# Optimization experiments

Measured on AMD Instinct MI355X. Metric: run time of the kernel, lower is better.

The kernel has to match this reference:

```python
import jax, jax.numpy as jnp
import numpy as np

B, T, D, H = 32, 1024, 1024, 1024


def gru_cell(x, h, W_ih, W_hh, b_ih, b_hh):
    # torch.nn.GRUCell math; gate order (r, z, n)
    gi = x @ W_ih.T + b_ih          # [B, 3H]
    gh = h @ W_hh.T + b_hh          # [B, 3H]
    i_r, i_z, i_n = jnp.split(gi, 3, axis=-1)
    h_r, h_z, h_n = jnp.split(gh, 3, axis=-1)
    r = jax.nn.sigmoid(i_r + h_r)
    z = jax.nn.sigmoid(i_z + h_z)
    n = jnp.tanh(i_n + r * h_n)
    return (1.0 - z) * n + z * h


def setup_inputs() -> dict:
    key = jax.random.key(0)
    k = jax.random.split(key, 6)
    scale = np.float32(1.0 / np.sqrt(H))  # torch GRUCell init range
    x = jax.random.normal(k[0], (B, T, D), jnp.float32)
    seg = jax.random.randint(k[1], (B, T), 0, 2).astype(jnp.int32)
    W_ih = jax.random.normal(k[2], (3 * H, D), jnp.float32) * scale
    W_hh = jax.random.normal(k[3], (3 * H, H), jnp.float32) * scale
    b_ih = jax.random.normal(k[4], (3 * H,), jnp.float32) * scale
    b_hh = jax.random.normal(k[5], (3 * H,), jnp.float32) * scale
    return {"x": x, "W_ih": W_ih, "W_hh": W_hh, "b_ih": b_ih, "b_hh": b_hh, "seg": seg}


def reference(x, W_ih, W_hh, b_ih, b_hh, seg):
    # apply_rnn_pack: GRUCell scan with segment-masked reset + ragged pack.
    segf = seg.astype(x.dtype)

    def step(h, inp):
        xt, st = inp                      # xt [B,D], st [B]
        h_new = gru_cell(xt, h, W_ih, W_hh, b_ih, b_hh)
        h_next = st[:, None] * h_new      # reset hidden where seg==0
        return h_next, h_new              # emit pre-reset hidden

    h0 = jnp.zeros((B, H), x.dtype)
    xs = (jnp.swapaxes(x, 0, 1), jnp.swapaxes(segf, 0, 1))
    _, hs = jax.lax.scan(step, h0, xs)    # hs [T,B,H]
    hs = jnp.swapaxes(hs, 0, 1)           # [B,T,H]

    # Pack: write h at step t into slot (#emits before t) iff seg[b,t]==0.
    emit = seg == 0                       # [B,T]
    pos = jnp.cumsum(emit, axis=1) - 1    # destination slot for emitted steps
    pos = jnp.where(emit, pos, T)         # route non-emitted steps to pad slot
    out = jnp.zeros((B, T + 1, H), x.dtype)
    b_idx = jnp.arange(B)[:, None]
    out = out.at[b_idx, pos].set(hs)
    out = out[:, :T]                      # [B,T,H], ragged-padded with zeros
    counts = emit.sum(axis=1)             # per-sample packed lengths (idx)
    return out, counts
```

## Files before the change

### kernel.cpp

```cpp
#include <hip/hip_runtime.h>

#define NB 32
#define NT 1024
#define ND 1024
#define NH 1024
#define G3 3072
#define MROWS 32768
#define HROWS 16512
#define GSROWS 32896
#define TAILG 256

typedef __bf16 bf16x8 __attribute__((ext_vector_type(8)));
typedef float f32x4 __attribute__((ext_vector_type(4)));
typedef unsigned short u16x8 __attribute__((ext_vector_type(8)));
typedef unsigned short u16x4 __attribute__((ext_vector_type(4)));

__device__ __forceinline__ float b2f(unsigned short u){
  union { unsigned int i; float f; } v; v.i = ((unsigned int)u) << 16; return v.f;
}
__device__ __forceinline__ unsigned short f2b(float f){
  union { float f; unsigned int i; } v; v.f = f;
  unsigned int r = (v.i + 0x7FFFu + ((v.i >> 16) & 1u)) >> 16;
  return (unsigned short)r;
}
__device__ __forceinline__ float sigm(float x){ return 1.0f / (1.0f + __expf(-x)); }
__device__ __forceinline__ float tanh_(float x){ return 2.0f / (1.0f + __expf(-2.0f * x)) - 1.0f; }

__device__ __forceinline__ void g2l16(const void* g, void* l){
  __builtin_amdgcn_global_load_lds((__attribute__((address_space(1))) void*)g,
                                   (__attribute__((address_space(3))) void*)l, 16, 0, 0);
}

__global__ __launch_bounds__(256) void k_setup(const float* __restrict__ wih,
    const float* __restrict__ whh, const float* __restrict__ x,
    unsigned short* __restrict__ wih_b, unsigned short* __restrict__ whh_b,
    unsigned short* __restrict__ x_b, int has_xb, f32x4* __restrict__ outv, int out_n4){
  int i0 = blockIdx.x * 256 + threadIdx.x;
  int stride = gridDim.x * 256;
  f32x4 z = {0.f, 0.f, 0.f, 0.f};
  for (int j = i0; j < out_n4; j += stride) __builtin_nontemporal_store(z, &outv[j]);
  int nw4 = (G3 * ND) / 4;
  for (int j = i0; j < nw4; j += stride){
    f32x4 a = ((const f32x4*)wih)[j];
    f32x4 b = ((const f32x4*)whh)[j];
    u16x4 ua = {f2b(a[0]), f2b(a[1]), f2b(a[2]), f2b(a[3])};
    u16x4 ub = {f2b(b[0]), f2b(b[1]), f2b(b[2]), f2b(b[3])};
    ((u16x4*)wih_b)[j] = ua;
    ((u16x4*)whh_b)[j] = ub;
  }
  if (has_xb){
    int nx4 = (MROWS * ND) / 4;
    for (int j = i0; j < nx4; j += stride){
      f32x4 a = ((const f32x4*)x)[j];
      u16x4 u = {f2b(a[0]), f2b(a[1]), f2b(a[2]), f2b(a[3])};
      ((u16x4*)x_b)[j] = u;
    }
  }
}

__global__ __launch_bounds__(1024) void k_segbuild(const int* __restrict__ seg,
    int* __restrict__ ugi, int* __restrict__ uout, int* __restrict__ ulen,
    int* __restrict__ nseg_b,
    int* __restrict__ sgi, int* __restrict__ sout, int* __restrict__ slen,
    int* __restrict__ cnt_ge, int* __restrict__ base_g,
    unsigned int* __restrict__ perm, unsigned int* __restrict__ bar,
    float* __restrict__ counts_out){
  __shared__ int hist[1025];
  __shared__ int sufx[1024];
  __shared__ int pref[1024];
  __shared__ int offs[1025];
  int tid = threadIdx.x;
  int wave = tid >> 6, lane = tid & 63;
  if (tid == 0) *bar = 0u;

  for (int b = wave; b < NB; b += 16){
    int prev = -1;
    int zc = 0;
    for (int c = 0; c < 16; ++c){
      int t = c * 64 + lane;
      int v = seg[b * NT + t];
      unsigned long long mask = __ballot(v == 0);
      unsigned long long below = mask & ((1ULL << lane) - 1ULL);
      if (v == 0){
        int pz = below ? (c * 64 + (63 - __clzll((long long)below))) : prev;
        int eidx = zc + __popcll(below);
        int slot = b * NT + eidx;
        ugi[slot]  = b * NT + (pz + 1);
        uout[slot] = b * NT + eidx;
        ulen[slot] = t - pz;
      }
      if (mask) prev = c * 64 + (63 - __clzll((long long)mask));
      zc += __popcll(mask);
    }
    if (lane == 0){ nseg_b[b] = zc; counts_out[b] = (float)zc; }
  }
  __syncthreads();
  for (int i = tid; i <= 1024; i += 1024) hist[i] = 0;
  __syncthreads();
  for (int s = tid; s < NB * NT; s += 1024){
    int b = s >> 10, j = s & 1023;
    if (j < nseg_b[b]) atomicAdd(&hist[ulen[s]], 1);
  }
  __syncthreads();
  if (tid < 1024) sufx[tid] = hist[tid + 1];
  __syncthreads();
  for (int off = 1; off < 1024; off <<= 1){
    int v = (tid + off < 1024) ? sufx[tid + off] : 0;
    __syncthreads();
    sufx[tid] += v;
    __syncthreads();
  }
  cnt_ge[tid + 1] = sufx[tid];
  if (tid == 0){ cnt_ge[0] = sufx[0]; cnt_ge[1025] = 0; }
  offs[tid] = sufx[tid];
  if (tid == 0) offs[1024] = 0;
  pref[tid] = sufx[tid];
  __syncthreads();
  for (int off = 1; off < 1024; off <<= 1){
    int v = (tid >= off) ? pref[tid - off] : 0;
    __syncthreads();
    pref[tid] += v;
    __syncthreads();
  }
  base_g[tid + 1] = pref[tid];
  if (tid == 0){ base_g[0] = 0; base_g[1025] = pref[1023]; }
  __syncthreads();
  for (int s = tid; s < NB * NT; s += 1024){
    int b = s >> 10, j = s & 1023;
    if (j < nseg_b[b]){
      int len = ulen[s];
      int p = atomicAdd(&offs[len], 1);
      sgi[p] = ugi[s]; sout[p] = uout[s]; slen[p] = len;
    }
  }
  for (int m = tid; m < MROWS; m += 1024) perm[m] = 0xFFFFFFFFu;
  __syncthreads();
  int nseg = cnt_ge[1];
  for (int p = tid; p < nseg; p += 1024){
    int src = sgi[p];
    int len = slen[p];
    perm[src] = (unsigned int)p;
    for (int kk = 1; kk < len; ++kk)
      perm[src + kk] = (unsigned int)(pref[kk - 1] + p);
  }
}

__global__ __launch_bounds__(256, 2) void k_gi_gemm(const float* __restrict__ x,
    const unsigned short* __restrict__ x_b, const unsigned short* __restrict__ wih_b,
    const float* __restrict__ b_ih, const unsigned int* __restrict__ perm,
    unsigned short* __restrict__ gs, int use_xb){
  __shared__ unsigned short Alds[128 * 64];
  __shared__ unsigned short Blds[128 * 64];
  int tid = threadIdx.x;
  int w = tid >> 6, lane = tid & 63;
  int mtile = blockIdx.x / 24, ntile = blockIdx.x % 24;
  int m0 = mtile * 128, n0 = ntile * 128;
  int mh = (w >> 1) * 64, nh = (w & 1) * 64;
  int lrow = lane >> 3;
  int lcol = 8 * ((lane & 7) ^ lrow);
  f32x4 acc[4][4];
#pragma unroll
  for (int i = 0; i < 4; ++i)
#pragma unroll
    for (int j = 0; j < 4; ++j) acc[i][j] = (f32x4){0.f, 0.f, 0.f, 0.f};

  for (int kc = 0; kc < 16; ++kc){
    __syncthreads();
    if (use_xb){
#pragma unroll
      for (int p = 0; p < 4; ++p){
        int s = w * 4 + p;
        g2l16(x_b + (size_t)(m0 + s * 8 + lrow) * ND + kc * 64 + lcol, &Alds[s * 512]);
      }
    } else {
#pragma unroll
      for (int p = 0; p < 4; ++p){
        int e = (p * 256 + tid) * 8;
        int r = e >> 6, c = e & 63;
        const float* src = x + (size_t)(m0 + r) * ND + kc * 64 + c;
        f32x4 f0 = *(const f32x4*)src;
        f32x4 f1 = *(const f32x4*)(src + 4);
        u16x8 u;
        u[0]=f2b(f0[0]); u[1]=f2b(f0[1]); u[2]=f2b(f0[2]); u[3]=f2b(f0[3]);
        u[4]=f2b(f1[0]); u[5]=f2b(f1[1]); u[6]=f2b(f1[2]); u[7]=f2b(f1[3]);
        *(u16x8*)&Alds[r * 64 + (c ^ ((r & 7) << 3))] = u;
      }
    }
#pragma unroll
    for (int p = 0; p < 4; ++p){
      int s = w * 4 + p;
      g2l16(wih_b + (size_t)(n0 + s * 8 + lrow) * ND + kc * 64 + lcol, &Blds[s * 512]);
    }
    __syncthreads();
#pragma unroll
    for (int ks = 0; ks < 2; ++ks){
      int co = ks * 32 + (lane >> 4) * 8;
      int cx = co ^ ((lane & 7) << 3);
      bf16x8 a[4], bb[4];
#pragma unroll
      for (int mi = 0; mi < 4; ++mi)
        a[mi] = *(const bf16x8*)&Alds[(mh + mi * 16 + (lane & 15)) * 64 + cx];
#pragma unroll
      for (int ni = 0; ni < 4; ++ni)
        bb[ni] = *(const bf16x8*)&Blds[(nh + ni * 16 + (lane & 15)) * 64 + cx];
#pragma unroll
      for (int mi = 0; mi < 4; ++mi)
#pragma unroll
        for (int ni = 0; ni < 4; ++ni)
          acc[mi][ni] = __builtin_amdgcn_mfma_f32_16x16x32_bf16(a[mi], bb[ni], acc[mi][ni], 0, 0, 0);
    }
  }
#pragma unroll
  for (int mi = 0; mi < 4; ++mi){
    int rbase = m0 + mh + mi * 16 + (lane >> 4) * 4;
#pragma unroll
    for (int rr = 0; rr < 4; ++rr){
      unsigned int prow = perm[rbase + rr];
      if (prow == 0xFFFFFFFFu) continue;
#pragma unroll
      for (int ni = 0; ni < 4; ++ni){
        int col = n0 + nh + ni * 16 + (lane & 15);
        __builtin_nontemporal_store(f2b(acc[mi][ni][rr] + b_ih[col]),
                                    &gs[(size_t)prow * G3 + col]);
      }
    }
  }
}

__global__ __launch_bounds__(256) void k_step0(const float* __restrict__ b_hh,
    const unsigned short* __restrict__ gs,
    const int* __restrict__ sout, const int* __restrict__ cnt_ge,
    unsigned short* __restrict__ hbuf, float* __restrict__ out){
  int nseg = cnt_ge[1];
  int c2 = cnt_ge[2];
  int total = nseg * 128;
  for (int idx = blockIdx.x * 256 + threadIdx.x; idx < total; idx += gridDim.x * 256){
    int i = idx >> 7;
    int c0 = (idx & 127) * 8;
    bool emit = (i >= c2);
    const unsigned short* g = gs + (size_t)i * G3;
    u16x8 vr = __builtin_nontemporal_load((const u16x8*)(g + c0));
    u16x8 vz = __builtin_nontemporal_load((const u16x8*)(g + NH + c0));
    u16x8 vn = __builtin_nontemporal_load((const u16x8*)(g + 2 * NH + c0));
    float hn[8];
#pragma unroll
    for (int j = 0; j < 8; ++j){
      int c = c0 + j;
      float r = sigm(b2f(vr[j]) + b_hh[c]);
      float z = sigm(b2f(vz[j]) + b_hh[NH + c]);
      float n = tanh_(b2f(vn[j]) + r * b_hh[2 * NH + c]);
      hn[j] = (1.0f - z) * n;
    }
    if (emit){
      float* orow = out + (size_t)sout[i] * NH + c0;
      f32x4 v0 = {hn[0], hn[1], hn[2], hn[3]};
      f32x4 v1 = {hn[4], hn[5], hn[6], hn[7]};
      __builtin_nontemporal_store(v0, (f32x4*)orow);
      __builtin_nontemporal_store(v1, (f32x4*)(orow + 4));
    } else {
      u16x8 u;
#pragma unroll
      for (int j = 0; j < 8; ++j) u[j] = f2b(hn[j]);
      *(u16x8*)(hbuf + (size_t)HROWS * NH + (size_t)i * NH + c0) = u;
    }
  }
}

__device__ __forceinline__ void step_tile(int m0, int nc0, int Ak, int c2, int gbase,
    const unsigned short* __restrict__ whh_b, const float* __restrict__ b_hh,
    const unsigned short* __restrict__ gs, const int* __restrict__ sout,
    const unsigned short* __restrict__ hread, unsigned short* __restrict__ hwrite,
    float* __restrict__ out,
    unsigned short (*Alds)[64 * 128], unsigned short (*Blds)[192 * 128]){
  int tid = threadIdx.x;
  int w = tid >> 6, lane = tid & 63;
  int l15 = lane & 15, l4 = lane >> 4;

#define STAGE2(buf, kc) do {                                                        \
    _Pragma("unroll")                                                               \
    for (int p = 0; p < 4; ++p){                                                    \
      int s = w * 4 + p;                                                            \
      int ar = s * 4 + l4;                                                          \
      int sc = (l15 * 8) ^ ((ar & 7) << 3);                                         \
      g2l16(hread + (size_t)(m0 + ar) * NH + (kc) * 128 + sc, &Alds[buf][s * 512]); \
    }                                                                               \
    _Pragma("unroll")                                                               \
    for (int p = 0; p < 12; ++p){                                                   \
      int s = w * 12 + p;                                                           \
      int br = s * 4 + l4;                                                          \
      int wrow = (br >> 6) * NH + nc0 + (br & 63);                                  \
      int sc = (l15 * 8) ^ ((br & 7) << 3);                                         \
      g2l16(whh_b + (size_t)wrow * NH + (kc) * 128 + sc, &Blds[buf][s * 512]);      \
    }                                                                               \
  } while (0)

  STAGE2(0, 0);

  int c_lane = nc0 + w * 16 + l15;
  float bh_r = b_hh[c_lane], bh_z = b_hh[NH + c_lane], bh_n = b_hh[2 * NH + c_lane];
  unsigned short gr_[4][4], gz_[4][4], gn_[4][4], hv_[4][4];
  int so_[4][4];
#pragma unroll
  for (int a = 0; a < 4; ++a){
#pragma unroll
    for (int rr = 0; rr < 4; ++rr){
      int i = m0 + a * 16 + l4 * 4 + rr;
      const unsigned short* g = gs + (size_t)(gbase + i) * G3 + c_lane;
      gr_[a][rr] = __builtin_nontemporal_load(g);
      gz_[a][rr] = __builtin_nontemporal_load(g + NH);
      gn_[a][rr] = __builtin_nontemporal_load(g + 2 * NH);
      hv_[a][rr] = hread[(size_t)i * NH + c_lane];
      so_[a][rr] = sout[i < MROWS ? i : 0];
    }
  }

  f32x4 acc[4][3];
#pragma unroll
  for (int a = 0; a < 4; ++a)
#pragma unroll
    for (int b = 0; b < 3; ++b) acc[a][b] = (f32x4){0.f, 0.f, 0.f, 0.f};

  __syncthreads();
  int cur = 0;
  for (int kc = 0; kc < 8; ++kc){
    if (kc < 7) STAGE2(cur ^ 1, kc + 1);
#pragma unroll
    for (int ks = 0; ks < 4; ++ks){
      int co = ks * 32 + l4 * 8;
      bf16x8 av[4], bv[3];
#pragma unroll
      for (int a = 0; a < 4; ++a){
        int r = a * 16 + l15;
        av[a] = *(const bf16x8*)&Alds[cur][r * 128 + (co ^ ((r & 7) << 3))];
      }
#pragma unroll
      for (int b = 0; b < 3; ++b){
        int br = 64 * b + w * 16 + l15;
        bv[b] = *(const bf16x8*)&Blds[cur][br * 128 + (co ^ ((br & 7) << 3))];
      }
#pragma unroll
      for (int a = 0; a < 4; ++a)
#pragma unroll
        for (int b = 0; b < 3; ++b)
          acc[a][b] = __builtin_amdgcn_mfma_f32_16x16x32_bf16(av[a], bv[b], acc[a][b], 0, 0, 0);
    }
    __syncthreads();
    cur ^= 1;
  }
#undef STAGE2

#pragma unroll
  for (int a = 0; a < 4; ++a){
#pragma unroll
    for (int rr = 0; rr < 4; ++rr){
      int i = m0 + a * 16 + l4 * 4 + rr;
      if (i >= Ak) continue;
      bool emit = (i >= c2);
      float ghr = acc[a][0][rr] + bh_r;
      float ghz = acc[a][1][rr] + bh_z;
      float ghn = acc[a][2][rr] + bh_n;
      float h = b2f(hv_[a][rr]);
      float r = sigm(b2f(gr_[a][rr]) + ghr);
      float z = sigm(b2f(gz_[a][rr]) + ghz);
      float n = tanh_(b2f(gn_[a][rr]) + r * ghn);
      float hn = (1.0f - z) * n + z * h;
      if (emit) __builtin_nontemporal_store(hn, &out[(size_t)so_[a][rr] * NH + c_lane]);
      else      hwrite[(size_t)i * NH + c_lane] = f2b(hn);
    }
  }
}

__global__ __launch_bounds__(256, 1) void k_step(int k,
    const unsigned short* __restrict__ whh_b, const float* __restrict__ b_hh,
    const unsigned short* __restrict__ gs, const int* __restrict__ base_g,
    const int* __restrict__ sout, const int* __restrict__ cnt_ge,
    unsigned short* __restrict__ hbuf, float* __restrict__ out){
  __shared__ unsigned short Alds[2][64 * 128];
  __shared__ unsigned short Blds[2][192 * 128];
  int Ak = cnt_ge[k + 1];
  if (Ak <= 0) return;
  int c2 = cnt_ge[k + 2];
  int gbase = base_g[k];
  int Mt = (Ak + 63) >> 6;
  int tiles = Mt * 16;
  const unsigned short* hread = hbuf + (size_t)(k & 1) * HROWS * NH;
  unsigned short* hwrite      = hbuf + (size_t)((k + 1) & 1) * HROWS * NH;
  for (int t = blockIdx.x; t < tiles; t += gridDim.x){
    int cs = t & 15, mt = t >> 4;
    step_tile(mt * 64, cs * 64, Ak, c2, gbase, whh_b, b_hh, gs, sout,
              hread, hwrite, out, Alds, Blds);
  }
}

__global__ __launch_bounds__(256, 1) void k_tail(
    const unsigned short* __restrict__ whh_b, const float* __restrict__ b_hh,
    const unsigned short* __restrict__ gs, const int* __restrict__ base_g,
    const int* __restrict__ sout, const int* __restrict__ cnt_ge,
    unsigned short* __restrict__ hbuf, float* __restrict__ out,
    unsigned int* __restrict__ bar){
  __shared__ unsigned short Wlds[48 * 1024];
  int tid = threadIdx.x;
  int w = tid >> 6, lane = tid & 63;
  int l15 = lane & 15, l4 = lane >> 4;
  int cs = blockIdx.x & 63;
  int rg = blockIdx.x >> 6;

#pragma unroll
  for (int p = 0; p < 24; ++p){
    int s = w * 24 + p;
    int r = s >> 1, h = s & 1;
    int grow = (r >> 4) * NH + cs * 16 + (r & 15);
    int cp = h * 512 + lane * 8;
    g2l16(whh_b + (size_t)grow * NH + (cp ^ ((r & 7) << 3)),
          &Wlds[r * 1024 + h * 512 + lane * 8]);
  }
  __syncthreads();

  int c_lane = cs * 16 + l15;
  float bh_r = b_hh[c_lane], bh_z = b_hh[NH + c_lane], bh_n = b_hh[2 * NH + c_lane];

  unsigned int phase = 0;
  for (int k = 5; k <= 1023; ++k){
    int Ak = cnt_ge[k + 1];
    if (Ak <= 0) break;
    int c2 = cnt_ge[k + 2];
    int gbase = base_g[k];
    int Mt16 = (Ak + 15) >> 4;
    const unsigned short* hread = hbuf + (size_t)(k & 1) * HROWS * NH;
    unsigned short* hwrite      = hbuf + (size_t)((k + 1) & 1) * HROWS * NH;

    for (int mt = rg * 4 + w; mt < Mt16; mt += 16){
      int m0 = mt * 16;
      unsigned short gr_[4], gz_[4], gn_[4], hv_[4];
      int so_[4];
#pragma unroll
      for (int rr = 0; rr < 4; ++rr){
        int i = m0 + l4 * 4 + rr;
        const unsigned short* g = gs + (size_t)(gbase + i) * G3 + c_lane;
        gr_[rr] = __builtin_nontemporal_load(g);
        gz_[rr] = __builtin_nontemporal_load(g + NH);
        gn_[rr] = __builtin_nontemporal_load(g + 2 * NH);
        hv_[rr] = hread[(size_t)i * NH + c_lane];
        so_[rr] = sout[i < MROWS ? i : 0];
      }

      const unsigned short* arow = hread + (size_t)(m0 + l15) * NH + l4 * 8;
      f32x4 acc0 = {0.f, 0.f, 0.f, 0.f}, acc1 = acc0, acc2 = acc0;
#pragma unroll 4
      for (int ks = 0; ks < 32; ++ks){
        int co = ks * 32 + l4 * 8;
        bf16x8 a  = *(const bf16x8*)(arow + ks * 32);
        bf16x8 b0 = *(const bf16x8*)&Wlds[(0 * 16 + l15) * 1024 + (co ^ ((l15 & 7) << 3))];
        bf16x8 b1 = *(const bf16x8*)&Wlds[(1 * 16 + l15) * 1024 + (co ^ ((l15 & 7) << 3))];
        bf16x8 b2 = *(const bf16x8*)&Wlds[(2 * 16 + l15) * 1024 + (co ^ ((l15 & 7) << 3))];
        acc0 = __builtin_amdgcn_mfma_f32_16x16x32_bf16(a, b0, acc0, 0, 0, 0);
        acc1 = __builtin_amdgcn_mfma_f32_16x16x32_bf16(a, b1, acc1, 0, 0, 0);
        acc2 = __builtin_amdgcn_mfma_f32_16x16x32_bf16(a, b2, acc2, 0, 0, 0);
      }

#pragma unroll
      for (int rr = 0; rr < 4; ++rr){
        int i = m0 + l4 * 4 + rr;
        if (i >= Ak) continue;
        bool emit = (i >= c2);
        float h = b2f(hv_[rr]);
        float r = sigm(b2f(gr_[rr]) + acc0[rr] + bh_r);
        float z = sigm(b2f(gz_[rr]) + acc1[rr] + bh_z);
        float n = tanh_(b2f(gn_[rr]) + r * (acc2[rr] + bh_n));
        float hn = (1.0f - z) * n + z * h;
        if (emit) __builtin_nontemporal_store(hn, &out[(size_t)so_[rr] * NH + c_lane]);
        else      hwrite[(size_t)i * NH + c_lane] = f2b(hn);
      }
    }

    ++phase;
    __syncthreads();
    if (threadIdx.x == 0){
      __threadfence();
      atomicAdd(bar, 1u);
      unsigned int goal = phase * (unsigned int)TAILG;
      while (__hip_atomic_load(bar, __ATOMIC_RELAXED, __HIP_MEMORY_SCOPE_AGENT) < goal)
        __builtin_amdgcn_s_sleep(4);
      __threadfence();
    }
    __syncthreads();
  }
}

extern "C" void kernel_launch(void* const* d_in, const int* in_sizes, int n_in,
                              void* d_out, int out_size, void* d_ws, size_t ws_size,
                              hipStream_t stream){
  (void)in_sizes; (void)n_in;
  const float* x   = (const float*)d_in[0];
  const float* wih = (const float*)d_in[1];
  const float* whh = (const float*)d_in[2];
  const float* bih = (const float*)d_in[3];
  const float* bhh = (const float*)d_in[4];
  const int*   seg = (const int*)d_in[5];
  float* outp = (float*)d_out;

  char* ws = (char*)d_ws;
  size_t o_wih = 0;
  size_t o_whh = 6291456;
  size_t o_gs  = 12582912;
  size_t o_desc = o_gs + (size_t)GSROWS * G3 * 2;
  size_t o_h    = o_desc + (2u << 20);
  size_t o_xb   = o_h + (size_t)2 * HROWS * NH * 2;
  size_t need_xb = o_xb + (size_t)MROWS * ND * 2;
  int has_xb = (ws_size >= need_xb) ? 1 : 0;

  unsigned short* wih_b = (unsigned short*)(ws + o_wih);
  unsigned short* whh_b = (unsigned short*)(ws + o_whh);
  unsigned short* gsort = (unsigned short*)(ws + o_gs);
  int* ugi  = (int*)(ws + o_desc);
  int* uout = ugi + 32768;
  int* ulen = uout + 32768;
  int* sgi  = ulen + 32768;
  int* sout = sgi + 32768;
  int* slen = sout + 32768;
  int* nsegb = slen + 32768;
  int* cntge = nsegb + 64;
  int* baseg = cntge + 1056;
  unsigned int* perm = (unsigned int*)(baseg + 1056);
  unsigned int* bar  = perm + MROWS;
  unsigned short* hbuf = (unsigned short*)(ws + o_h);
  unsigned short* x_b  = (unsigned short*)(ws + o_xb);

  float* counts_out = outp + (size_t)NB * NT * NH;
  int out_n4 = out_size / 4;

  k_setup<<<dim3(4096), dim3(256), 0, stream>>>(wih, whh, x, wih_b, whh_b, x_b, has_xb,
                                                (f32x4*)d_out, out_n4);

  k_segbuild<<<dim3(1), dim3(1024), 0, stream>>>(seg, ugi, uout, ulen, nsegb,
                                                 sgi, sout, slen, cntge, baseg,
                                                 perm, bar, counts_out);

  k_gi_gemm<<<dim3(256 * 24), dim3(256), 0, stream>>>(x, x_b, wih_b, bih, perm, gsort, has_xb);

  k_step0<<<dim3(1024), dim3(256), 0, stream>>>(bhh, gsort, sout, cntge, hbuf, outp);

  static const int grids[5] = {0, 1024, 1024, 512, 256};
  for (int k = 1; k <= 4; ++k){
    k_step<<<dim3(grids[k]), dim3(256), 0, stream>>>(k, whh_b, bhh, gsort, baseg,
                                                     sout, cntge, hbuf, outp);
  }

  k_tail<<<dim3(TAILG), dim3(256), 0, stream>>>(whh_b, bhh, gsort, baseg,
                                                sout, cntge, hbuf, outp, bar);
}
```

Before: 1.068 ms.

## Shrink tail grid to 64 blocks and replace fences with agent-scope atomic loads/stores

The persistent tail kernel now runs 64 blocks, one per column slice, instead of 256, so each grid barrier has fewer participants. Each block's 4 waves cover all row tiles. The __threadfence calls around the barrier are removed. Hidden-state reads and writes now use relaxed agent-scope atomic loads and stores so other CUs see them without a full fence. The inner loop unroll is raised to 8. The trade is less parallelism per step in exchange for cheaper synchronisation. Correctness now depends on relaxed atomics plus the atomicAdd giving enough ordering, which is a memory-model risk.

```diff
diff --git a/kernel.cpp b/kernel.cpp
--- a/kernel.cpp
+++ b/kernel.cpp
@@ -8,7 +8,7 @@
 #define MROWS 32768
 #define HROWS 16512
 #define GSROWS 32896
-#define TAILG 256
+#define TAILG 64
 
 typedef __bf16 bf16x8 __attribute__((ext_vector_type(8)));
 typedef float f32x4 __attribute__((ext_vector_type(4)));
@@ -29,6 +29,17 @@
 __device__ __forceinline__ void g2l16(const void* g, void* l){
   __builtin_amdgcn_global_load_lds((__attribute__((address_space(1))) void*)g,
                                    (__attribute__((address_space(3))) void*)l, 16, 0, 0);
+}
+
+__device__ __forceinline__ unsigned long long ld_agent_u64(const unsigned short* p){
+  return __hip_atomic_load((const unsigned long long*)p, __ATOMIC_RELAXED,
+                           __HIP_MEMORY_SCOPE_AGENT);
+}
+__device__ __forceinline__ unsigned short ld_agent_u16(const unsigned short* p){
+  return __hip_atomic_load(p, __ATOMIC_RELAXED, __HIP_MEMORY_SCOPE_AGENT);
+}
+__device__ __forceinline__ void st_agent_u16(unsigned short* p, unsigned short v){
+  __hip_atomic_store(p, v, __ATOMIC_RELAXED, __HIP_MEMORY_SCOPE_AGENT);
 }
 
 __global__ __launch_bounds__(256) void k_setup(const float* __restrict__ wih,
@@ -402,8 +413,7 @@
   int tid = threadIdx.x;
   int w = tid >> 6, lane = tid & 63;
   int l15 = lane & 15, l4 = lane >> 4;
-  int cs = blockIdx.x & 63;
-  int rg = blockIdx.x >> 6;
+  int cs = blockIdx.x;
 
 #pragma unroll
   for (int p = 0; p < 24; ++p){
@@ -429,7 +439,7 @@
     const unsigned short* hread = hbuf + (size_t)(k & 1) * HROWS * NH;
     unsigned short* hwrite      = hbuf + (size_t)((k + 1) & 1) * HROWS * NH;
 
-    for (int mt = rg * 4 + w; mt < Mt16; mt += 16){
+    for (int mt = w; mt < Mt16; mt += 4){
       int m0 = mt * 16;
       unsigned short gr_[4], gz_[4], gn_[4], hv_[4];
       int so_[4];
@@ -440,22 +450,25 @@
         gr_[rr] = __builtin_nontemporal_load(g);
         gz_[rr] = __builtin_nontemporal_load(g + NH);
         gn_[rr] = __builtin_nontemporal_load(g + 2 * NH);
-        hv_[rr] = hread[(size_t)i * NH + c_lane];
+        hv_[rr] = ld_agent_u16(hread + (size_t)i * NH + c_lane);
         so_[rr] = sout[i < MROWS ? i : 0];
       }
 
       const unsigned short* arow = hread + (size_t)(m0 + l15) * NH + l4 * 8;
       f32x4 acc0 = {0.f, 0.f, 0.f, 0.f}, acc1 = acc0, acc2 = acc0;
-#pragma unroll 4
+#pragma unroll 8
       for (int ks = 0; ks < 32; ++ks){
         int co = ks * 32 + l4 * 8;
-        bf16x8 a  = *(const bf16x8*)(arow + ks * 32);
-        bf16x8 b0 = *(const bf16x8*)&Wlds[(0 * 16 + l15) * 1024 + (co ^ ((l15 & 7) << 3))];
-        bf16x8 b1 = *(const bf16x8*)&Wlds[(1 * 16 + l15) * 1024 + (co ^ ((l15 & 7) << 3))];
-        bf16x8 b2 = *(const bf16x8*)&Wlds[(2 * 16 + l15) * 1024 + (co ^ ((l15 & 7) << 3))];
-        acc0 = __builtin_amdgcn_mfma_f32_16x16x32_bf16(a, b0, acc0, 0, 0, 0);
-        acc1 = __builtin_amdgcn_mfma_f32_16x16x32_bf16(a, b1, acc1, 0, 0, 0);
-        acc2 = __builtin_amdgcn_mfma_f32_16x16x32_bf16(a, b2, acc2, 0, 0, 0);
+        union { bf16x8 v; unsigned long long q[2]; } a;
+        a.q[0] = ld_agent_u64(arow + ks * 32);
+        a.q[1] = ld_agent_u64(arow + ks * 32 + 4);
+        int cx = co ^ ((l15 & 7) << 3);
+        bf16x8 b0 = *(const bf16x8*)&Wlds[(0 * 16 + l15) * 1024 + cx];
+        bf16x8 b1 = *(const bf16x8*)&Wlds[(1 * 16 + l15) * 1024 + cx];
+        bf16x8 b2 = *(const bf16x8*)&Wlds[(2 * 16 + l15) * 1024 + cx];
+        acc0 = __builtin_amdgcn_mfma_f32_16x16x32_bf16(a.v, b0, acc0, 0, 0, 0);
+        acc1 = __builtin_amdgcn_mfma_f32_16x16x32_bf16(a.v, b1, acc1, 0, 0, 0);
+        acc2 = __builtin_amdgcn_mfma_f32_16x16x32_bf16(a.v, b2, acc2, 0, 0, 0);
       }
 
 #pragma unroll
@@ -469,19 +482,17 @@
         float n = tanh_(b2f(gn_[rr]) + r * (acc2[rr] + bh_n));
         float hn = (1.0f - z) * n + z * h;
         if (emit) __builtin_nontemporal_store(hn, &out[(size_t)so_[rr] * NH + c_lane]);
-        else      hwrite[(size_t)i * NH + c_lane] = f2b(hn);
+        else      st_agent_u16(hwrite + (size_t)i * NH + c_lane, f2b(hn));
       }
     }
 
     ++phase;
     __syncthreads();
     if (threadIdx.x == 0){
-      __threadfence();
       atomicAdd(bar, 1u);
       unsigned int goal = phase * (unsigned int)TAILG;
       while (__hip_atomic_load(bar, __ATOMIC_RELAXED, __HIP_MEMORY_SCOPE_AGENT) < goal)
-        __builtin_amdgcn_s_sleep(4);
-      __threadfence();
+        __builtin_amdgcn_s_sleep(2);
     }
     __syncthreads();
   }
```

After: 1.005 ms. 5.9% less time.
